# Optimization experiments

Measured on AMD Instinct MI355X. Metric: run time of the kernel, lower is better.

## Reference

```python
import jax, jax.numpy as jnp
import numpy as np

B, V, L = 256, 128000, 2048
EPS = 1e-05


def setup_inputs() -> dict:
    key = jax.random.key(0)
    k1, k2, k3, k4, k5 = jax.random.split(key, 5)
    logits_next = jax.random.normal(k1, (B, V), jnp.float32)
    token_ids = jax.random.randint(k2, (B, L), 0, V, jnp.int32)
    presence_penalties = jax.random.uniform(k3, (B,), jnp.float32) * 1.5
    temperatures = jax.random.uniform(k4, (B,), jnp.float32, 0.5, 1.5)
    # make first quarter of the batch greedy (temperature == 0)
    temperatures = temperatures.at[: B // 4].set(0.0)
    u = jax.random.uniform(k5, (B, V), jnp.float32, 1e-9, 1.0)
    gumbel = -jnp.log(-jnp.log(u))  # Gumbel(0,1) noise for multinomial sampling
    return {
        "logits_next": logits_next,
        "token_ids": token_ids,
        "presence_penalties": presence_penalties,
        "temperatures": temperatures,
        "gumbel": gumbel,
    }


def reference(logits_next, token_ids, presence_penalties, temperatures, gumbel):
    Bn, Vn = logits_next.shape
    # presence mask: 1.0 where token id appeared in the history (counts > 0)
    rows = jnp.arange(Bn, dtype=jnp.int32)[:, None]  # [B,1]
    presence = jnp.zeros((Bn, Vn), logits_next.dtype).at[rows, token_ids].set(1.0)
    penalized = logits_next - presence_penalties[:, None] * presence

    greedy = temperatures < EPS  # [B]
    safe_t = jnp.where(greedy, jnp.float32(1.0), temperatures)
    scaled = penalized / safe_t[:, None]

    # greedy rows: plain argmax; sample rows: Gumbel-max == multinomial(softmax)
    greedy_tok = jnp.argmax(penalized, axis=-1)
    sampled_tok = jnp.argmax(scaled + gumbel, axis=-1)
    token_ids_next = jnp.where(greedy, greedy_tok, sampled_tok)
    return token_ids_next.astype(jnp.int32)
```

## Files before the change

kernel.cpp:

```cpp
#include <hip/hip_runtime.h>
#include <math.h>

#define BATCH 256
#define VOCAB 128000
#define HIST  2048
#define EPS_T 1e-5f

#define BBLOCK 256
#define BLOCKS_PER_ROW 8
#define GRID (BATCH * BLOCKS_PER_ROW)
#define WAVES_PER_ROW (BLOCKS_PER_ROW * 4)
#define CHUNKS (VOCAB / 256)
#define MASK_WORDS (VOCAB / 32)

typedef float f32x4 __attribute__((ext_vector_type(4)));

__device__ __forceinline__ unsigned fkey(float f) {
    unsigned b = __float_as_uint(f);
    return (b & 0x80000000u) ? ~b : (b | 0x80000000u);
}

__device__ __forceinline__ void upd(float s, int idx, float& best, int& besti) {
    if (s > best || (s == best && idx < besti)) { best = s; besti = idx; }
}

__device__ __forceinline__ void body4(f32x4 l, unsigned w, int sh, float pen,
                                      int idx0, float& best, int& besti) {
    #pragma unroll
    for (int j = 0; j < 4; j++) {
        float present = (float)((w >> (sh + j)) & 1u);
        float p = l[j] - pen * present;
        upd(p, idx0 + j, best, besti);
    }
}

__device__ __forceinline__ void body4s(f32x4 l, f32x4 g, unsigned w, int sh,
                                       float pen, float temp,
                                       int idx0, float& best, int& besti) {
    #pragma unroll
    for (int j = 0; j < 4; j++) {
        float present = (float)((w >> (sh + j)) & 1u);
        float p = l[j] - pen * present;
        float s = p / temp + g[j];
        upd(s, idx0 + j, best, besti);
    }
}

__global__ __launch_bounds__(BBLOCK, 1) void fused_scan(
    const float* __restrict__ logits,
    const float* __restrict__ gumbel,
    const int*   __restrict__ token_ids,
    const float* __restrict__ penalties,
    const float* __restrict__ temps,
    unsigned long long* __restrict__ keys)
{
    __shared__ unsigned smask[MASK_WORDS];

    const int blk  = blockIdx.x;
    const int row  = blk >> 3;
    const int tid  = threadIdx.x;
    const int lane = tid & 63;
    const int wave = tid >> 6;
    const int wir  = ((blk & 7) << 2) | wave;

    const float pen    = penalties[row];
    const float temp   = temps[row];
    const bool  greedy = (temp < EPS_T);

    const int4* rt = (const int4*)(token_ids + (size_t)row * HIST);
    int4 ta = rt[tid];
    int4 tb = rt[tid + BBLOCK];

    for (int i = tid; i < MASK_WORDS; i += BBLOCK) smask[i] = 0u;
    __syncthreads();

    atomicOr(&smask[ta.x >> 5], 1u << (ta.x & 31));
    atomicOr(&smask[ta.y >> 5], 1u << (ta.y & 31));
    atomicOr(&smask[ta.z >> 5], 1u << (ta.z & 31));
    atomicOr(&smask[ta.w >> 5], 1u << (ta.w & 31));
    atomicOr(&smask[tb.x >> 5], 1u << (tb.x & 31));
    atomicOr(&smask[tb.y >> 5], 1u << (tb.y & 31));
    atomicOr(&smask[tb.z >> 5], 1u << (tb.z & 31));
    atomicOr(&smask[tb.w >> 5], 1u << (tb.w & 31));
    __syncthreads();

    const f32x4* Lr = (const f32x4*)(logits + (size_t)row * VOCAB);
    const f32x4* Gr = (const f32x4*)(gumbel + (size_t)row * VOCAB);

    float best  = -INFINITY;
    int   besti = 0x7fffffff;
    const int sh    = (lane & 7) * 4;
    const int wsub  = lane >> 3;

    if (greedy) {
        int c = wir;
        f32x4 lc = __builtin_nontemporal_load(Lr + c * 64 + lane);
        while (true) {
            const int cn = c + 32;
            f32x4 ln = lc;
            if (cn < CHUNKS) ln = __builtin_nontemporal_load(Lr + cn * 64 + lane);
            const unsigned w = smask[c * 8 + wsub];
            body4(lc, w, sh, pen, c * 256 + lane * 4, best, besti);
            if (cn >= CHUNKS) break;
            lc = ln; c = cn;
        }
    } else {
        int c = wir;
        f32x4 lc = __builtin_nontemporal_load(Lr + c * 64 + lane);
        f32x4 gc = __builtin_nontemporal_load(Gr + c * 64 + lane);
        while (true) {
            const int cn = c + 32;
            f32x4 ln = lc, gn = gc;
            if (cn < CHUNKS) {
                ln = __builtin_nontemporal_load(Lr + cn * 64 + lane);
                gn = __builtin_nontemporal_load(Gr + cn * 64 + lane);
            }
            const unsigned w = smask[c * 8 + wsub];
            body4s(lc, gc, w, sh, pen, temp, c * 256 + lane * 4, best, besti);
            if (cn >= CHUNKS) break;
            lc = ln; gc = gn; c = cn;
        }
    }

    #pragma unroll
    for (int off = 32; off > 0; off >>= 1) {
        float ov = __shfl_down(best, off, 64);
        int   oi = __shfl_down(besti, off, 64);
        if (ov > best || (ov == best && oi < besti)) { best = ov; besti = oi; }
    }

    if (lane == 0) {
        unsigned long long key =
            ((unsigned long long)fkey(best) << 32) | (unsigned)(~besti);
        atomicMax(keys + row, key);
    }
}

__global__ void decode_kernel(const unsigned long long* __restrict__ keys,
                              int* __restrict__ out)
{
    const int b = threadIdx.x;
    out[b] = (int)(~(unsigned)keys[b]);
}

extern "C" void kernel_launch(void* const* d_in, const int* in_sizes, int n_in,
                              void* d_out, int out_size, void* d_ws, size_t ws_size,
                              hipStream_t stream) {
    const float* logits    = (const float*)d_in[0];
    const int*   token_ids = (const int*)d_in[1];
    const float* penalties = (const float*)d_in[2];
    const float* temps     = (const float*)d_in[3];
    const float* gumbel    = (const float*)d_in[4];
    int* out = (int*)d_out;

    unsigned long long* keys = (unsigned long long*)d_ws;

    hipMemsetAsync(keys, 0, BATCH * sizeof(unsigned long long), stream);

    fused_scan<<<GRID, BBLOCK, 0, stream>>>(logits, gumbel, token_ids,
                                            penalties, temps, keys);
    decode_kernel<<<1, BATCH, 0, stream>>>(keys, out);
}
```

Baseline: 252.4 us.

## Deepen load prefetch, fuse decode into scan via completion counter, relax launch bounds

The scan loops now keep two chunks in flight instead of one, which adds memory-level parallelism to a bandwidth-bound streaming argmax. The separate decode kernel is removed: the last wave to finish a row, detected with a per-row atomic counter, writes the output token, which saves one kernel launch. Launch bounds allow 8 blocks per CU, and the per-element tie-break comparison is simplified to a strict greater-than. Within a thread indices are visited in increasing order, so the simpler comparison still keeps the first index on ties. Raising the occupancy hint may constrain register allocation.

```diff
diff --git a/kernel.cpp b/kernel.cpp
--- a/kernel.cpp
+++ b/kernel.cpp
@@ -21,7 +21,7 @@
 }
 
 __device__ __forceinline__ void upd(float s, int idx, float& best, int& besti) {
-    if (s > best || (s == best && idx < besti)) { best = s; besti = idx; }
+    if (s > best) { best = s; besti = idx; }
 }
 
 __device__ __forceinline__ void body4(f32x4 l, unsigned w, int sh, float pen,
@@ -46,13 +46,15 @@
     }
 }
 
-__global__ __launch_bounds__(BBLOCK, 1) void fused_scan(
+__global__ __launch_bounds__(BBLOCK, 8) void fused_scan(
     const float* __restrict__ logits,
     const float* __restrict__ gumbel,
     const int*   __restrict__ token_ids,
     const float* __restrict__ penalties,
     const float* __restrict__ temps,
-    unsigned long long* __restrict__ keys)
+    unsigned long long* __restrict__ keys,
+    unsigned int* __restrict__ cnt,
+    int* __restrict__ out)
 {
     __shared__ unsigned smask[MASK_WORDS];
 
@@ -93,32 +95,47 @@
     const int wsub  = lane >> 3;
 
     if (greedy) {
-        int c = wir;
+        int c  = wir;
+        int c1 = c + 32;
         f32x4 lc = __builtin_nontemporal_load(Lr + c * 64 + lane);
+        f32x4 ln{};
+        bool has1 = (c1 < CHUNKS);
+        if (has1) ln = __builtin_nontemporal_load(Lr + c1 * 64 + lane);
         while (true) {
-            const int cn = c + 32;
-            f32x4 ln = lc;
-            if (cn < CHUNKS) ln = __builtin_nontemporal_load(Lr + cn * 64 + lane);
+            const int c2 = c + 64;
+            const bool has2 = (c2 < CHUNKS);
+            f32x4 l2{};
+            if (has2) l2 = __builtin_nontemporal_load(Lr + c2 * 64 + lane);
             const unsigned w = smask[c * 8 + wsub];
             body4(lc, w, sh, pen, c * 256 + lane * 4, best, besti);
-            if (cn >= CHUNKS) break;
-            lc = ln; c = cn;
+            if (!has1) break;
+            lc = ln; c = c1;
+            ln = l2; c1 = c2; has1 = has2;
         }
     } else {
-        int c = wir;
+        int c  = wir;
+        int c1 = c + 32;
         f32x4 lc = __builtin_nontemporal_load(Lr + c * 64 + lane);
         f32x4 gc = __builtin_nontemporal_load(Gr + c * 64 + lane);
+        f32x4 ln{}, gn{};
+        bool has1 = (c1 < CHUNKS);
+        if (has1) {
+            ln = __builtin_nontemporal_load(Lr + c1 * 64 + lane);
+            gn = __builtin_nontemporal_load(Gr + c1 * 64 + lane);
+        }
         while (true) {
-            const int cn = c + 32;
-            f32x4 ln = lc, gn = gc;
-            if (cn < CHUNKS) {
-                ln = __builtin_nontemporal_load(Lr + cn * 64 + lane);
-                gn = __builtin_nontemporal_load(Gr + cn * 64 + lane);
+            const int c2 = c + 64;
+            const bool has2 = (c2 < CHUNKS);
+            f32x4 l2{}, g2{};
+            if (has2) {
+                l2 = __builtin_nontemporal_load(Lr + c2 * 64 + lane);
+                g2 = __builtin_nontemporal_load(Gr + c2 * 64 + lane);
             }
             const unsigned w = smask[c * 8 + wsub];
             body4s(lc, gc, w, sh, pen, temp, c * 256 + lane * 4, best, besti);
-            if (cn >= CHUNKS) break;
-            lc = ln; gc = gn; c = cn;
+            if (!has1) break;
+            lc = ln; gc = gn; c = c1;
+            ln = l2; gn = g2; c1 = c2; has1 = has2;
         }
     }
 
@@ -133,14 +150,13 @@
         unsigned long long key =
             ((unsigned long long)fkey(best) << 32) | (unsigned)(~besti);
         atomicMax(keys + row, key);
+        __threadfence();
+        unsigned done = atomicAdd(cnt + row, 1u);
+        if (done == WAVES_PER_ROW - 1) {
+            unsigned long long fin = atomicMax(keys + row, 0ull);
+            out[row] = (int)(~(unsigned)fin);
+        }
     }
-}
-
-__global__ void decode_kernel(const unsigned long long* __restrict__ keys,
-                              int* __restrict__ out)
-{
-    const int b = threadIdx.x;
-    out[b] = (int)(~(unsigned)keys[b]);
 }
 
 extern "C" void kernel_launch(void* const* d_in, const int* in_sizes, int n_in,
@@ -154,10 +170,12 @@
     int* out = (int*)d_out;
 
     unsigned long long* keys = (unsigned long long*)d_ws;
+    unsigned int*       cnt  = (unsigned int*)(keys + BATCH);
 
-    hipMemsetAsync(keys, 0, BATCH * sizeof(unsigned long long), stream);
+    hipMemsetAsync(d_ws, 0,
+                   BATCH * (sizeof(unsigned long long) + sizeof(unsigned int)),
+                   stream);
 
     fused_scan<<<GRID, BBLOCK, 0, stream>>>(logits, gumbel, token_ids,
-                                            penalties, temps, keys);
-    decode_kernel<<<1, BATCH, 0, stream>>>(keys, out);
+                                            penalties, temps, keys, cnt, out);
 }
```

Result: slower. 528.9 us (+109.5%).

## Give each wave a contiguous chunk range and simplify the per-element argmax compare

Applied to the files above, without the earlier changes.

Each wave now scans a contiguous block of 256-element chunks instead of a strided set of chunks spaced 32 apart. The conditional loop exit becomes a fixed-count loop with a peeled final iteration. Because each lane now sees indices in increasing order, the per-element tie-break on index is dropped and only a strict greater-than compare is used. The aim is more sequential DRAM access per wave and fewer compare instructions. In exchange, the mask reads and block placement across a row change.

```diff
diff --git a/kernel.cpp b/kernel.cpp
--- a/kernel.cpp
+++ b/kernel.cpp
@@ -9,9 +9,10 @@
 #define BBLOCK 256
 #define BLOCKS_PER_ROW 8
 #define GRID (BATCH * BLOCKS_PER_ROW)
-#define WAVES_PER_ROW (BLOCKS_PER_ROW * 4)
 #define CHUNKS (VOCAB / 256)
 #define MASK_WORDS (VOCAB / 32)
+#define BASE_CH (CHUNKS / 32)
+#define EXTRA_W (CHUNKS - 32 * BASE_CH)
 
 typedef float f32x4 __attribute__((ext_vector_type(4)));
 
@@ -21,7 +22,7 @@
 }
 
 __device__ __forceinline__ void upd(float s, int idx, float& best, int& besti) {
-    if (s > best || (s == best && idx < besti)) { best = s; besti = idx; }
+    if (s > best) { best = s; besti = idx; }
 }
 
 __device__ __forceinline__ void body4(f32x4 l, unsigned w, int sh, float pen,
@@ -92,34 +93,33 @@
     const int sh    = (lane & 7) * 4;
     const int wsub  = lane >> 3;
 
+    const int n  = BASE_CH + (wir < EXTRA_W ? 1 : 0);
+    const int c0 = wir * BASE_CH + (wir < EXTRA_W ? wir : EXTRA_W);
+
     if (greedy) {
-        int c = wir;
-        f32x4 lc = __builtin_nontemporal_load(Lr + c * 64 + lane);
-        while (true) {
-            const int cn = c + 32;
-            f32x4 ln = lc;
-            if (cn < CHUNKS) ln = __builtin_nontemporal_load(Lr + cn * 64 + lane);
+        int c = c0;
+        f32x4 lc = __builtin_nontemporal_load(Lr + (size_t)c * 64 + lane);
+        for (int i = 1; i < n; ++i) {
+            f32x4 ln = __builtin_nontemporal_load(Lr + (size_t)(c0 + i) * 64 + lane);
             const unsigned w = smask[c * 8 + wsub];
             body4(lc, w, sh, pen, c * 256 + lane * 4, best, besti);
-            if (cn >= CHUNKS) break;
-            lc = ln; c = cn;
+            lc = ln; c = c0 + i;
         }
+        const unsigned w = smask[c * 8 + wsub];
+        body4(lc, w, sh, pen, c * 256 + lane * 4, best, besti);
     } else {
-        int c = wir;
-        f32x4 lc = __builtin_nontemporal_load(Lr + c * 64 + lane);
-        f32x4 gc = __builtin_nontemporal_load(Gr + c * 64 + lane);
-        while (true) {
-            const int cn = c + 32;
-            f32x4 ln = lc, gn = gc;
-            if (cn < CHUNKS) {
-                ln = __builtin_nontemporal_load(Lr + cn * 64 + lane);
-                gn = __builtin_nontemporal_load(Gr + cn * 64 + lane);
-            }
+        int c = c0;
+        f32x4 lc = __builtin_nontemporal_load(Lr + (size_t)c * 64 + lane);
+        f32x4 gc = __builtin_nontemporal_load(Gr + (size_t)c * 64 + lane);
+        for (int i = 1; i < n; ++i) {
+            f32x4 ln = __builtin_nontemporal_load(Lr + (size_t)(c0 + i) * 64 + lane);
+            f32x4 gn = __builtin_nontemporal_load(Gr + (size_t)(c0 + i) * 64 + lane);
             const unsigned w = smask[c * 8 + wsub];
             body4s(lc, gc, w, sh, pen, temp, c * 256 + lane * 4, best, besti);
-            if (cn >= CHUNKS) break;
-            lc = ln; gc = gn; c = cn;
+            lc = ln; gc = gn; c = c0 + i;
         }
+        const unsigned w = smask[c * 8 + wsub];
+        body4s(lc, gc, w, sh, pen, temp, c * 256 + lane * 4, best, besti);
     }
 
     #pragma unroll
```

New measurement: 253.5 us. About the same (+0.4%).
